# Kernel tuning notes

Measured on AMD Instinct MI355X. Metric: run time of the kernel, lower is better.

The kernel has to match this reference:

```python
import jax, jax.numpy as jnp
import numpy as np

N_NODES = 50000
N_EDGES = 800000
IN_FEATS = 128
OUT_FEATS = 128
ALPHA = 0.5
BETA = 0.5


def setup_inputs() -> dict:
    key = jax.random.key(0)
    k_feat, k_src, k_dst, k_w = jax.random.split(key, 4)
    feat = jax.random.normal(k_feat, (N_NODES, IN_FEATS), dtype=jnp.float32)
    src = jax.random.randint(k_src, (N_EDGES,), 0, N_NODES, dtype=jnp.int64)
    dst = jax.random.randint(k_dst, (N_EDGES,), 0, N_NODES, dtype=jnp.int64)
    # xavier_uniform init for weight, zeros for bias
    bound = float(np.sqrt(6.0 / (IN_FEATS + OUT_FEATS)))
    weight = jax.random.uniform(k_w, (IN_FEATS, OUT_FEATS), dtype=jnp.float32,
                                minval=-bound, maxval=bound)
    bias = jnp.zeros((OUT_FEATS,), dtype=jnp.float32)
    return {"feat": feat, "weight": weight, "bias": bias, "src": src, "dst": dst}


def reference(feat, weight, bias, src, dst):
    n = feat.shape[0]
    ones = jnp.ones(src.shape[0], dtype=feat.dtype)
    deg_out = jax.ops.segment_sum(ones, src, num_segments=n)  # out-degree per node
    deg_in = jax.ops.segment_sum(ones, dst, num_segments=n)   # in-degree per node
    deg_out = jnp.maximum(deg_out, 1.0)
    deg_in = jnp.maximum(deg_in, 1.0)
    # norm = deg_in^{-alpha} * deg_out^{-beta}, applied to source features
    norm = deg_in ** (-ALPHA) * deg_out ** (-BETA)  # [N]
    h = feat * norm[:, None]                        # [N, in]
    if IN_FEATS > OUT_FEATS:
        h = h @ weight                              # project first, then aggregate
        rst = jax.ops.segment_sum(h[src], dst, num_segments=n)
    else:
        rst = jax.ops.segment_sum(h[src], dst, num_segments=n)  # copy_u + sum SpMM
        rst = rst @ weight
    rst = rst + bias
    return jax.nn.relu(rst)
```

## Files before the change

kernel.cpp:

```cpp
#include <hip/hip_runtime.h>

#define NF 128
#define NCHUNK 32
#define NRH 4
#define NRF 8
#define NNW_MAX 25088
#define RWH_MAX ((NNW_MAX + NRH - 1) / NRH)
#define RWF_MAX ((NNW_MAX + NRF - 1) / NRF)
#define GG_NODES 16

typedef __attribute__((ext_vector_type(8))) short short8;
typedef __attribute__((ext_vector_type(4))) float f32x4;
typedef unsigned int uint;
typedef unsigned short ushort;

__device__ __forceinline__ ushort f2bf(float f) {
    uint u = __float_as_uint(f);
    uint r = (u + 0x7fffu + ((u >> 16) & 1u)) >> 16;
    return (ushort)r;
}
__device__ __forceinline__ float bflo(uint v) { return __uint_as_float(v << 16); }
__device__ __forceinline__ float bfhi(uint v) { return __uint_as_float(v & 0xffff0000u); }

__global__ __launch_bounds__(1024) void hist_kernel(const int* __restrict__ src,
                                                    const int* __restrict__ dst,
                                                    uint* __restrict__ partial_in,
                                                    uint* __restrict__ partial_out,
                                                    int n_edges, int nwords, int epb, int rw) {
    __shared__ uint h[RWH_MAX];
    int wbeg = blockIdx.z * rw;
    int wend = min(wbeg + rw, nwords);
    int nw = wend - wbeg;
    for (int w = threadIdx.x; w < nw; w += 1024) h[w] = 0;
    __syncthreads();
    const int* idx = blockIdx.y ? src : dst;
    int ebeg = blockIdx.x * epb;
    int eend = min(ebeg + epb, n_edges);
    int nodelo = wbeg * 2, nodehi = wend * 2;
    for (int e = ebeg + (int)threadIdx.x; e < eend; e += 1024) {
        int node = idx[e];
        if (node >= nodelo && node < nodehi)
            atomicAdd(&h[(node >> 1) - wbeg], 1u << ((node & 1) * 16));
    }
    __syncthreads();
    uint* p = (blockIdx.y ? partial_out : partial_in) + (size_t)blockIdx.x * nwords + wbeg;
    for (int w = threadIdx.x; w < nw; w += 1024) p[w] = h[w];
}

__global__ __launch_bounds__(512) void dnr_kernel(const uint* __restrict__ partial_in,
                                                  uint* __restrict__ partial_out,
                                                  int* __restrict__ deg_in,
                                                  float* __restrict__ norm,
                                                  int* __restrict__ bsum,
                                                  int nwords, int n) {
    int w = blockIdx.x * 512 + (int)threadIdx.x;
    uint si0 = 0, si1 = 0, so0 = 0, so1 = 0;
    if (w < nwords) {
        for (int c = 0; c < NCHUNK; ++c) {
            uint vi = partial_in[(size_t)c * nwords + w];
            uint vo = partial_out[(size_t)c * nwords + w];
            partial_out[(size_t)c * nwords + w] = si0 | (si1 << 16);
            si0 += vi & 0xffffu; si1 += vi >> 16;
            so0 += vo & 0xffffu; so1 += vo >> 16;
        }
        int n0 = 2 * w, n1 = 2 * w + 1;
        {
            uint di = si0 < 1u ? 1u : si0, dv = so0 < 1u ? 1u : so0;
            deg_in[n0] = (int)si0;
            norm[n0] = 1.0f / sqrtf((float)di * (float)dv);
        }
        if (n1 < n) {
            uint di = si1 < 1u ? 1u : si1, dv = so1 < 1u ? 1u : so1;
            deg_in[n1] = (int)si1;
            norm[n1] = 1.0f / sqrtf((float)di * (float)dv);
        }
    }
    int v = (int)(si0 + si1);
#pragma unroll
    for (int off = 32; off >= 1; off >>= 1) v += __shfl_down(v, off, 64);
    __shared__ int wsum[8];
    int wave = threadIdx.x >> 6, lane = threadIdx.x & 63;
    if (lane == 0) wsum[wave] = v;
    __syncthreads();
    if (threadIdx.x == 0) {
        int s = 0;
#pragma unroll
        for (int k = 0; k < 8; ++k) s += wsum[k];
        bsum[blockIdx.x] = s;
    }
}

__global__ __launch_bounds__(1024) void prepscan_kernel(const float* __restrict__ feat,
                                                        const float* __restrict__ norm,
                                                        uint* __restrict__ featn, int total,
                                                        const float* __restrict__ W,
                                                        uint* __restrict__ wt,
                                                        const int* __restrict__ deg,
                                                        const int* __restrict__ bsum,
                                                        int* __restrict__ start,
                                                        int n, int nb, int nfb4) {
    int bid = (int)blockIdx.x;
    if (bid < nfb4) {
        int idx = bid * 1024 + (int)threadIdx.x;
        if (idx < total) {
            int node = idx >> 6;
            float nv = norm[node];
            float2 v = ((const float2*)feat)[idx];
            featn[idx] = (uint)f2bf(v.x * nv) | ((uint)f2bf(v.y * nv) << 16);
        }
        return;
    }
    if (bid < nfb4 + 8) {
        int idx = (bid - nfb4) * 1024 + (int)threadIdx.x;
        if (idx < NF * NF / 2) {
            int nrow = idx >> 6;
            int k2 = idx & 63;
            float a = W[(2 * k2) * NF + nrow];
            float b = W[(2 * k2 + 1) * NF + nrow];
            wt[idx] = (uint)f2bf(a) | ((uint)f2bf(b) << 16);
        }
        return;
    }
    int b = bid - nfb4 - 8;
    if (b >= nb) return;
    __shared__ int ws[16];
    __shared__ int wo[16];
    __shared__ int bpre_s;
    int i = b * 1024 + (int)threadIdx.x;
    int v = (i < n) ? deg[i] : 0;
    int lane = threadIdx.x & 63, wv = threadIdx.x >> 6;
    int incl = v;
#pragma unroll
    for (int off = 1; off < 64; off <<= 1) {
        int t = __shfl_up(incl, off, 64);
        if (lane >= off) incl += t;
    }
    if (lane == 63) ws[wv] = incl;
    if (threadIdx.x < 64) {
        int bb = ((int)threadIdx.x < nb) ? bsum[threadIdx.x] : 0;
        int bi = bb;
#pragma unroll
        for (int off = 1; off < 64; off <<= 1) {
            int t = __shfl_up(bi, off, 64);
            if (lane >= off) bi += t;
        }
        int bex = bi - bb;
        int mine = __shfl(bex, b, 64);
        if (threadIdx.x == 0) bpre_s = mine;
    }
    __syncthreads();
    if (threadIdx.x == 0) {
        int s = 0;
#pragma unroll
        for (int k = 0; k < 16; ++k) { wo[k] = s; s += ws[k]; }
    }
    __syncthreads();
    if (i < n) start[i] = incl - v + wo[wv] + bpre_s;
}

__global__ __launch_bounds__(1024) void fill3_kernel(const int* __restrict__ src,
                                                     const int* __restrict__ dst,
                                                     const uint* __restrict__ rel,
                                                     const int* __restrict__ start,
                                                     int* __restrict__ csr_src,
                                                     int n_edges, int nwords, int epb, int rwf) {
    __shared__ uint cur[RWF_MAX];
    int c = blockIdx.x >> 3;
    int r = blockIdx.x & 7;
    int wbeg = r * rwf;
    int wend = min(wbeg + rwf, nwords);
    int nw = wend - wbeg;
    for (int w = threadIdx.x; w < nw; w += 1024) cur[w] = 0;
    __syncthreads();
    const uint* relc = rel + (size_t)c * nwords;
    int ebeg = c * epb;
    int eend = min(ebeg + epb, n_edges);
    int nodelo = wbeg * 2, nodehi = wend * 2;
    for (int e = ebeg + (int)threadIdx.x; e < eend; e += 1024) {
        int d = dst[e];
        if (d >= nodelo && d < nodehi) {
            int sh = (d & 1) * 16;
            uint old = atomicAdd(&cur[(d >> 1) - wbeg], 1u << sh);
            uint rank = (old >> sh) & 0xffffu;
            uint relv = (relc[d >> 1] >> sh) & 0xffffu;
            int pos = start[d] + (int)(relv + rank);
            csr_src[pos] = src[e];
        }
    }
}

__global__ __launch_bounds__(128) void gathergemm_kernel(const uint* __restrict__ featn,
                                                         const int* __restrict__ csr_src,
                                                         const int* __restrict__ start,
                                                         const int* __restrict__ deg,
                                                         const ushort* __restrict__ wt_h,
                                                         const float* __restrict__ bias,
                                                         float* __restrict__ out,
                                                         int n_nodes) {
    __shared__ uint rstl[GG_NODES][68];
    int wave = threadIdx.x >> 6;
    int lane = threadIdx.x & 63;
    int base = blockIdx.x * GG_NODES;
    if (base >= n_nodes) return;
    int half = lane >> 5;
    int hl   = lane & 31;

    for (int p = 0; p < 4; ++p) {
        int node = base + wave * 8 + p * 2 + half;
        int beg = 0, dg = 0;
        if (node < n_nodes) { beg = start[node]; dg = deg[node]; }
        const uint2* fp = (const uint2*)featn;
        float a0x = 0.f, a0y = 0.f, a1x = 0.f, a1y = 0.f;
        float b0x = 0.f, b0y = 0.f, b1x = 0.f, b1y = 0.f;
        int i = 0;
        for (; i + 7 < dg; i += 8) {
            int s0 = csr_src[beg + i];
            int s1 = csr_src[beg + i + 1];
            int s2 = csr_src[beg + i + 2];
            int s3 = csr_src[beg + i + 3];
            int s4 = csr_src[beg + i + 4];
            int s5 = csr_src[beg + i + 5];
            int s6 = csr_src[beg + i + 6];
            int s7 = csr_src[beg + i + 7];
            uint2 v0 = fp[(size_t)s0 * 32 + hl];
            uint2 v1 = fp[(size_t)s1 * 32 + hl];
            uint2 v2 = fp[(size_t)s2 * 32 + hl];
            uint2 v3 = fp[(size_t)s3 * 32 + hl];
            uint2 v4 = fp[(size_t)s4 * 32 + hl];
            uint2 v5 = fp[(size_t)s5 * 32 + hl];
            uint2 v6 = fp[(size_t)s6 * 32 + hl];
            uint2 v7 = fp[(size_t)s7 * 32 + hl];
            a0x += bflo(v0.x); a0y += bfhi(v0.x); a1x += bflo(v0.y); a1y += bfhi(v0.y);
            b0x += bflo(v1.x); b0y += bfhi(v1.x); b1x += bflo(v1.y); b1y += bfhi(v1.y);
            a0x += bflo(v2.x); a0y += bfhi(v2.x); a1x += bflo(v2.y); a1y += bfhi(v2.y);
            b0x += bflo(v3.x); b0y += bfhi(v3.x); b1x += bflo(v3.y); b1y += bfhi(v3.y);
            a0x += bflo(v4.x); a0y += bfhi(v4.x); a1x += bflo(v4.y); a1y += bfhi(v4.y);
            b0x += bflo(v5.x); b0y += bfhi(v5.x); b1x += bflo(v5.y); b1y += bfhi(v5.y);
            a0x += bflo(v6.x); a0y += bfhi(v6.x); a1x += bflo(v6.y); a1y += bfhi(v6.y);
            b0x += bflo(v7.x); b0y += bfhi(v7.x); b1x += bflo(v7.y); b1y += bfhi(v7.y);
        }
        for (; i + 1 < dg; i += 2) {
            int s0 = csr_src[beg + i];
            int s1 = csr_src[beg + i + 1];
            uint2 v0 = fp[(size_t)s0 * 32 + hl];
            uint2 v1 = fp[(size_t)s1 * 32 + hl];
            a0x += bflo(v0.x); a0y += bfhi(v0.x); a1x += bflo(v0.y); a1y += bfhi(v0.y);
            b0x += bflo(v1.x); b0y += bfhi(v1.x); b1x += bflo(v1.y); b1y += bfhi(v1.y);
        }
        if (i < dg) {
            int s = csr_src[beg + i];
            uint2 v = fp[(size_t)s * 32 + hl];
            a0x += bflo(v.x); a0y += bfhi(v.x); a1x += bflo(v.y); a1y += bfhi(v.y);
        }
        float r0x = a0x + b0x, r0y = a0y + b0y;
        float r1x = a1x + b1x, r1y = a1y + b1y;
        uint w0 = (uint)f2bf(r0x) | ((uint)f2bf(r0y) << 16);
        uint w1 = (uint)f2bf(r1x) | ((uint)f2bf(r1y) << 16);
        *(uint2*)&rstl[wave * 8 + p * 2 + half][hl * 2] = make_uint2(w0, w1);
    }
    __syncthreads();

    int l16 = lane & 15, lq = lane >> 4;
    int nt0 = wave * 4;

    short8 a[4];
#pragma unroll
    for (int kt = 0; kt < 4; ++kt)
        a[kt] = *(const short8*)&rstl[l16][kt * 16 + lq * 4];

#pragma unroll
    for (int t = 0; t < 4; ++t) {
        int nt = nt0 + t;
        f32x4 acc = {0.0f, 0.0f, 0.0f, 0.0f};
        const ushort* bp = wt_h + (size_t)(nt * 16 + l16) * NF + lq * 8;
#pragma unroll
        for (int kt = 0; kt < 4; ++kt) {
            short8 b = *(const short8*)(bp + kt * 32);
            acc = __builtin_amdgcn_mfma_f32_16x16x32_bf16(a[kt], b, acc, 0, 0, 0);
        }
        int col = nt * 16 + l16;
        float bv = bias[col];
#pragma unroll
        for (int r = 0; r < 4; ++r) {
            int orow = base + lq * 4 + r;
            if (orow < n_nodes) {
                float v = acc[r] + bv;
                out[(size_t)orow * NF + col] = v > 0.0f ? v : 0.0f;
            }
        }
    }
}

__global__ __launch_bounds__(256) void deg_kernel(const int* __restrict__ src,
                                                  const int* __restrict__ dst,
                                                  int* __restrict__ deg_out,
                                                  int* __restrict__ deg_in,
                                                  int n_edges) {
    int i = blockIdx.x * 256 + threadIdx.x;
    if (i < n_edges) {
        atomicAdd(&deg_out[src[i]], 1);
        atomicAdd(&deg_in[dst[i]], 1);
    }
}
__global__ __launch_bounds__(256) void norm_kernel(const int* __restrict__ deg_out,
                                                   const int* __restrict__ deg_in,
                                                   float* __restrict__ norm, int n) {
    int i = blockIdx.x * 256 + threadIdx.x;
    if (i < n) {
        int dov = deg_out[i]; if (dov < 1) dov = 1;
        int div_ = deg_in[i]; if (div_ < 1) div_ = 1;
        norm[i] = 1.0f / sqrtf((float)dov * (float)div_);
    }
}
__global__ __launch_bounds__(256) void prep_kernel(const float* __restrict__ feat,
                                                   const float* __restrict__ norm,
                                                   uint* __restrict__ featn, int total,
                                                   const float* __restrict__ W,
                                                   uint* __restrict__ wt, int nfb) {
    if ((int)blockIdx.x < nfb) {
        int idx = blockIdx.x * 256 + threadIdx.x;
        if (idx >= total) return;
        int node = idx >> 6;
        float nv = norm[node];
        float2 v = ((const float2*)feat)[idx];
        featn[idx] = (uint)f2bf(v.x * nv) | ((uint)f2bf(v.y * nv) << 16);
    } else {
        int idx = (blockIdx.x - nfb) * 256 + threadIdx.x;
        if (idx >= NF * NF / 2) return;
        int nrow = idx >> 6;
        int k2 = idx & 63;
        float a = W[(2 * k2) * NF + nrow];
        float b = W[(2 * k2 + 1) * NF + nrow];
        wt[idx] = (uint)f2bf(a) | ((uint)f2bf(b) << 16);
    }
}
__global__ __launch_bounds__(1024) void scan_sum_kernel(const int* __restrict__ deg,
                                                        int* __restrict__ bsum, int n) {
    int i = blockIdx.x * 1024 + threadIdx.x;
    int v = (i < n) ? deg[i] : 0;
#pragma unroll
    for (int off = 32; off >= 1; off >>= 1) v += __shfl_down(v, off, 64);
    __shared__ int ws[16];
    int wv = threadIdx.x >> 6, lane = threadIdx.x & 63;
    if (lane == 0) ws[wv] = v;
    __syncthreads();
    if (threadIdx.x == 0) {
        int s = 0;
#pragma unroll
        for (int k = 0; k < 16; ++k) s += ws[k];
        bsum[blockIdx.x] = s;
    }
}
__global__ __launch_bounds__(1024) void scan_bsum_kernel(int* __restrict__ bsum, int nb) {
    __shared__ int s[1024];
    int v = (threadIdx.x < (unsigned)nb) ? bsum[threadIdx.x] : 0;
    s[threadIdx.x] = v;
    __syncthreads();
    for (int off = 1; off < 1024; off <<= 1) {
        int t = (threadIdx.x >= (unsigned)off) ? s[threadIdx.x - off] : 0;
        __syncthreads();
        s[threadIdx.x] += t;
        __syncthreads();
    }
    if (threadIdx.x < (unsigned)nb) bsum[threadIdx.x] = s[threadIdx.x] - v;
}
__global__ __launch_bounds__(1024) void scan_final_kernel(const int* __restrict__ deg,
                                                          const int* __restrict__ bsum,
                                                          int* __restrict__ start,
                                                          int* __restrict__ cursor, int n) {
    int i = blockIdx.x * 1024 + threadIdx.x;
    int v = (i < n) ? deg[i] : 0;
    int lane = threadIdx.x & 63, wv = threadIdx.x >> 6;
    int incl = v;
#pragma unroll
    for (int off = 1; off < 64; off <<= 1) {
        int t = __shfl_up(incl, off, 64);
        if (lane >= off) incl += t;
    }
    __shared__ int ws[16];
    __shared__ int wo[16];
    if (lane == 63) ws[wv] = incl;
    __syncthreads();
    if (threadIdx.x == 0) {
        int s = 0;
#pragma unroll
        for (int k = 0; k < 16; ++k) { wo[k] = s; s += ws[k]; }
    }
    __syncthreads();
    int excl = incl - v + wo[wv] + bsum[blockIdx.x];
    if (i < n) { start[i] = excl; cursor[i] = excl; }
}
__global__ __launch_bounds__(256) void fill_kernel(const int* __restrict__ src,
                                                   const int* __restrict__ dst,
                                                   int* __restrict__ cursor,
                                                   int* __restrict__ csr_src,
                                                   int n_edges) {
    int e = blockIdx.x * 256 + threadIdx.x;
    if (e < n_edges) {
        int d = dst[e];
        int pos = atomicAdd(&cursor[d], 1);
        csr_src[pos] = src[e];
    }
}
__global__ __launch_bounds__(256) void gather_kernel(const uint* __restrict__ featn,
                                                     const int* __restrict__ csr_src,
                                                     const int* __restrict__ start,
                                                     const int* __restrict__ deg,
                                                     uint* __restrict__ rst_h,
                                                     int n_nodes) {
    int wid  = (blockIdx.x * 256 + threadIdx.x) >> 6;
    int lane = threadIdx.x & 63;
    if (wid >= n_nodes) return;
    int beg = start[wid];
    int end = beg + deg[wid];
    float ax = 0.f, ay = 0.f;
    for (int i = beg; i < end; ++i) {
        int s = csr_src[i];
        uint v = featn[(size_t)s * 64 + lane];
        ax += bflo(v); ay += bfhi(v);
    }
    rst_h[(size_t)wid * 64 + lane] = (uint)f2bf(ax) | ((uint)f2bf(ay) << 16);
}
__global__ __launch_bounds__(256) void gemm_mfma_kernel(const ushort* __restrict__ rst_h,
                                                        const ushort* __restrict__ wt_h,
                                                        const float* __restrict__ bias,
                                                        float* __restrict__ out,
                                                        int n_nodes) {
    int wave = threadIdx.x >> 6;
    int lane = threadIdx.x & 63;
    int row0 = blockIdx.x * 64 + wave * 16;
    if (row0 >= n_nodes) return;
    int l16 = lane & 15, lq = lane >> 4;
    short8 a[4];
    const ushort* ap = rst_h + (size_t)(row0 + l16) * NF + lq * 8;
#pragma unroll
    for (int kt = 0; kt < 4; ++kt) a[kt] = *(const short8*)(ap + kt * 32);
#pragma unroll
    for (int nt = 0; nt < 8; ++nt) {
        f32x4 acc = {0.0f, 0.0f, 0.0f, 0.0f};
        const ushort* bp = wt_h + (size_t)(nt * 16 + l16) * NF + lq * 8;
#pragma unroll
        for (int kt = 0; kt < 4; ++kt) {
            short8 b = *(const short8*)(bp + kt * 32);
            acc = __builtin_amdgcn_mfma_f32_16x16x32_bf16(a[kt], b, acc, 0, 0, 0);
        }
        int col = nt * 16 + l16;
        float bv = bias[col];
#pragma unroll
        for (int r = 0; r < 4; ++r) {
            int orow = row0 + lq * 4 + r;
            if (orow < n_nodes) {
                float v = acc[r] + bv;
                out[(size_t)orow * NF + col] = v > 0.0f ? v : 0.0f;
            }
        }
    }
}

extern "C" void kernel_launch(void* const* d_in, const int* in_sizes, int n_in,
                              void* d_out, int out_size, void* d_ws, size_t ws_size,
                              hipStream_t stream) {
    const float* feat = (const float*)d_in[0];
    const float* W    = (const float*)d_in[1];
    const float* bias = (const float*)d_in[2];
    const int*   src  = (const int*)d_in[3];
    const int*   dst  = (const int*)d_in[4];

    int n_nodes = in_sizes[0] / NF;
    int n_edges = in_sizes[3];

    char* ws = (char*)d_ws;
    size_t row_u32 = (size_t)n_nodes * 64;
    uint*  rst_h   = (uint*)ws;
    uint*  featn   = rst_h + row_u32;
    int*   deg_in  = (int*)(featn + row_u32);
    int*   deg_out = deg_in + n_nodes;
    float* norm    = (float*)(deg_out + n_nodes);
    int*   start   = (int*)(norm + n_nodes);
    int*   cursor  = start + n_nodes;
    int*   bsum    = cursor + n_nodes;
    uint*  wt      = (uint*)(bsum + 1024);
    int*   csr_src = (int*)(wt + NF * NF / 2);
    uint*  partial_in = (uint*)(csr_src + n_edges);

    int nwords = (n_nodes + 1) / 2;
    uint* partial_out = partial_in + (size_t)NCHUNK * nwords;
    size_t need = (size_t)((char*)(partial_out + (size_t)NCHUNK * nwords) - ws);

    int epb = (n_edges + NCHUNK - 1) / NCHUNK;
    int nb1024 = (n_nodes + 1023) / 1024;
    bool fast = (nwords <= NNW_MAX) && (epb < 65536) && (nb1024 <= 64) && (need <= ws_size);

    int total = n_nodes * 64;

    if (fast) {
        int rwh = (nwords + NRH - 1) / NRH;
        hist_kernel<<<dim3(NCHUNK, 2, NRH), 1024, 0, stream>>>(
            src, dst, partial_in, partial_out, n_edges, nwords, epb, rwh);
        dnr_kernel<<<nb1024, 512, 0, stream>>>(partial_in, partial_out, deg_in, norm,
                                               bsum, nwords, n_nodes);
        int nfb4 = (total + 1023) / 1024;
        prepscan_kernel<<<nfb4 + 8 + nb1024, 1024, 0, stream>>>(
            feat, norm, featn, total, W, wt, deg_in, bsum, start, n_nodes, nb1024, nfb4);
        int rwf = (nwords + NRF - 1) / NRF;
        fill3_kernel<<<NCHUNK * NRF, 1024, 0, stream>>>(src, dst, partial_out, start,
                                                        csr_src, n_edges, nwords, epb, rwf);
        gathergemm_kernel<<<(n_nodes + GG_NODES - 1) / GG_NODES, 128, 0, stream>>>(
            featn, csr_src, start, deg_in, (const ushort*)wt, bias, (float*)d_out, n_nodes);
    } else {
        int nfb = (total + 255) / 256;
        hipMemsetAsync(deg_in, 0, 2 * (size_t)n_nodes * sizeof(int), stream);
        deg_kernel<<<(n_edges + 255) / 256, 256, 0, stream>>>(src, dst, deg_out, deg_in, n_edges);
        norm_kernel<<<(n_nodes + 255) / 256, 256, 0, stream>>>(deg_out, deg_in, norm, n_nodes);
        prep_kernel<<<nfb + 32, 256, 0, stream>>>(feat, norm, featn, total, W, wt, nfb);
        int nb = (n_nodes + 1023) / 1024;
        scan_sum_kernel<<<nb, 1024, 0, stream>>>(deg_in, bsum, n_nodes);
        scan_bsum_kernel<<<1, 1024, 0, stream>>>(bsum, nb);
        scan_final_kernel<<<nb, 1024, 0, stream>>>(deg_in, bsum, start, cursor, n_nodes);
        fill_kernel<<<(n_edges + 255) / 256, 256, 0, stream>>>(src, dst, cursor, csr_src, n_edges);
        gather_kernel<<<(n_nodes * 64 + 255) / 256, 256, 0, stream>>>(featn, csr_src, start,
                                                                      deg_in, rst_h, n_nodes);
        gemm_mfma_kernel<<<(n_nodes + 63) / 64, 256, 0, stream>>>((const ushort*)rst_h,
                                                                  (const ushort*)wt, bias,
                                                                  (float*)d_out, n_nodes);
    }
}
```

Before: 93.81 us.

## Slice feature columns into four planes and split fused gather-GEMM into two kernels

Stores the normalized bf16 features as four column-slice planes of 32 features each. The gather runs one block per tile/slice pair, and each half-wave handles alternate edges for a slice, combining the halves with a shuffle. The idea is to shrink the gathered working set per slice so it stays cache resident and to give the gather more parallelism. The fused GEMM is replaced by a separate MFMA GEMM kernel that reads the sliced aggregate from global memory, which adds an extra launch and an intermediate write and read.

```diff
diff --git a/kernel.cpp b/kernel.cpp
--- a/kernel.cpp
+++ b/kernel.cpp
@@ -7,7 +7,8 @@
 #define NNW_MAX 25088
 #define RWH_MAX ((NNW_MAX + NRH - 1) / NRH)
 #define RWF_MAX ((NNW_MAX + NRF - 1) / NRF)
-#define GG_NODES 16
+#define GT_NODES 16
+#define NSL 4
 
 typedef __attribute__((ext_vector_type(8))) short short8;
 typedef __attribute__((ext_vector_type(4))) float f32x4;
@@ -103,9 +104,13 @@
     if (bid < nfb4) {
         int idx = bid * 1024 + (int)threadIdx.x;
         if (idx < total) {
-            int node = idx >> 6;
+            int spn = n * 16;
+            int slice = idx / spn;
+            int rem = idx - slice * spn;
+            int node = rem >> 4;
+            int u = rem & 15;
             float nv = norm[node];
-            float2 v = ((const float2*)feat)[idx];
+            float2 v = ((const float2*)feat)[node * 64 + slice * 16 + u];
             featn[idx] = (uint)f2bf(v.x * nv) | ((uint)f2bf(v.y * nv) << 16);
         }
         return;
@@ -189,88 +194,77 @@
     }
 }
 
-__global__ __launch_bounds__(128) void gathergemm_kernel(const uint* __restrict__ featn,
-                                                         const int* __restrict__ csr_src,
-                                                         const int* __restrict__ start,
-                                                         const int* __restrict__ deg,
-                                                         const ushort* __restrict__ wt_h,
-                                                         const float* __restrict__ bias,
-                                                         float* __restrict__ out,
-                                                         int n_nodes) {
-    __shared__ uint rstl[GG_NODES][68];
+__global__ __launch_bounds__(128) void gather_sl_kernel(const uint* __restrict__ featn,
+                                                        const int* __restrict__ csr_src,
+                                                        const int* __restrict__ start,
+                                                        const int* __restrict__ deg,
+                                                        uint* __restrict__ rst_sl,
+                                                        int n_nodes, int ntiles) {
+    int q = blockIdx.x & 7;
+    int tile = (blockIdx.x >> 3) * 2 + (q >> 2);
+    int slice = q & 3;
+    if (tile >= ntiles) return;
     int wave = threadIdx.x >> 6;
     int lane = threadIdx.x & 63;
-    int base = blockIdx.x * GG_NODES;
-    if (base >= n_nodes) return;
     int half = lane >> 5;
-    int hl   = lane & 31;
+    int hl = lane & 31;
+    int epair = hl >> 4;
+    int l16 = hl & 15;
+    const uint* fs = featn + (size_t)slice * n_nodes * 16;
 
     for (int p = 0; p < 4; ++p) {
-        int node = base + wave * 8 + p * 2 + half;
+        int node = tile * GT_NODES + wave * 8 + p * 2 + half;
         int beg = 0, dg = 0;
         if (node < n_nodes) { beg = start[node]; dg = deg[node]; }
-        const uint2* fp = (const uint2*)featn;
-        float a0x = 0.f, a0y = 0.f, a1x = 0.f, a1y = 0.f;
-        float b0x = 0.f, b0y = 0.f, b1x = 0.f, b1y = 0.f;
-        int i = 0;
-        for (; i + 7 < dg; i += 8) {
+        float ax0 = 0.f, ay0 = 0.f, ax1 = 0.f, ay1 = 0.f;
+        int i = epair;
+        for (; i + 6 < dg; i += 8) {
             int s0 = csr_src[beg + i];
-            int s1 = csr_src[beg + i + 1];
-            int s2 = csr_src[beg + i + 2];
-            int s3 = csr_src[beg + i + 3];
-            int s4 = csr_src[beg + i + 4];
-            int s5 = csr_src[beg + i + 5];
-            int s6 = csr_src[beg + i + 6];
-            int s7 = csr_src[beg + i + 7];
-            uint2 v0 = fp[(size_t)s0 * 32 + hl];
-            uint2 v1 = fp[(size_t)s1 * 32 + hl];
-            uint2 v2 = fp[(size_t)s2 * 32 + hl];
-            uint2 v3 = fp[(size_t)s3 * 32 + hl];
-            uint2 v4 = fp[(size_t)s4 * 32 + hl];
-            uint2 v5 = fp[(size_t)s5 * 32 + hl];
-            uint2 v6 = fp[(size_t)s6 * 32 + hl];
-            uint2 v7 = fp[(size_t)s7 * 32 + hl];
-            a0x += bflo(v0.x); a0y += bfhi(v0.x); a1x += bflo(v0.y); a1y += bfhi(v0.y);
-            b0x += bflo(v1.x); b0y += bfhi(v1.x); b1x += bflo(v1.y); b1y += bfhi(v1.y);
-            a0x += bflo(v2.x); a0y += bfhi(v2.x); a1x += bflo(v2.y); a1y += bfhi(v2.y);
-            b0x += bflo(v3.x); b0y += bfhi(v3.x); b1x += bflo(v3.y); b1y += bfhi(v3.y);
-            a0x += bflo(v4.x); a0y += bfhi(v4.x); a1x += bflo(v4.y); a1y += bfhi(v4.y);
-            b0x += bflo(v5.x); b0y += bfhi(v5.x); b1x += bflo(v5.y); b1y += bfhi(v5.y);
-            a0x += bflo(v6.x); a0y += bfhi(v6.x); a1x += bflo(v6.y); a1y += bfhi(v6.y);
-            b0x += bflo(v7.x); b0y += bfhi(v7.x); b1x += bflo(v7.y); b1y += bfhi(v7.y);
-        }
-        for (; i + 1 < dg; i += 2) {
-            int s0 = csr_src[beg + i];
-            int s1 = csr_src[beg + i + 1];
-            uint2 v0 = fp[(size_t)s0 * 32 + hl];
-            uint2 v1 = fp[(size_t)s1 * 32 + hl];
-            a0x += bflo(v0.x); a0y += bfhi(v0.x); a1x += bflo(v0.y); a1y += bfhi(v0.y);
-            b0x += bflo(v1.x); b0y += bfhi(v1.x); b1x += bflo(v1.y); b1y += bfhi(v1.y);
-        }
-        if (i < dg) {
+            int s1 = csr_src[beg + i + 2];
+            int s2 = csr_src[beg + i + 4];
+            int s3 = csr_src[beg + i + 6];
+            uint v0 = fs[(size_t)s0 * 16 + l16];
+            uint v1 = fs[(size_t)s1 * 16 + l16];
+            uint v2 = fs[(size_t)s2 * 16 + l16];
+            uint v3 = fs[(size_t)s3 * 16 + l16];
+            ax0 += bflo(v0); ay0 += bfhi(v0);
+            ax1 += bflo(v1); ay1 += bfhi(v1);
+            ax0 += bflo(v2); ay0 += bfhi(v2);
+            ax1 += bflo(v3); ay1 += bfhi(v3);
+        }
+        for (; i < dg; i += 2) {
             int s = csr_src[beg + i];
-            uint2 v = fp[(size_t)s * 32 + hl];
-            a0x += bflo(v.x); a0y += bfhi(v.x); a1x += bflo(v.y); a1y += bfhi(v.y);
-        }
-        float r0x = a0x + b0x, r0y = a0y + b0y;
-        float r1x = a1x + b1x, r1y = a1y + b1y;
-        uint w0 = (uint)f2bf(r0x) | ((uint)f2bf(r0y) << 16);
-        uint w1 = (uint)f2bf(r1x) | ((uint)f2bf(r1y) << 16);
-        *(uint2*)&rstl[wave * 8 + p * 2 + half][hl * 2] = make_uint2(w0, w1);
-    }
-    __syncthreads();
-
+            uint v = fs[(size_t)s * 16 + l16];
+            ax0 += bflo(v); ay0 += bfhi(v);
+        }
+        float ax = ax0 + ax1, ay = ay0 + ay1;
+        ax += __shfl_xor(ax, 16, 64);
+        ay += __shfl_xor(ay, 16, 64);
+        if (epair == 0 && node < n_nodes)
+            rst_sl[((size_t)slice * n_nodes + node) * 16 + l16] =
+                (uint)f2bf(ax) | ((uint)f2bf(ay) << 16);
+    }
+}
+
+__global__ __launch_bounds__(256) void gemm_sl_kernel(const ushort* __restrict__ rst_sl,
+                                                      const ushort* __restrict__ wt_h,
+                                                      const float* __restrict__ bias,
+                                                      float* __restrict__ out,
+                                                      int n_nodes) {
+    int wave = threadIdx.x >> 6;
+    int lane = threadIdx.x & 63;
+    int row0 = blockIdx.x * 64 + wave * 16;
+    if (row0 >= n_nodes) return;
     int l16 = lane & 15, lq = lane >> 4;
-    int nt0 = wave * 4;
+    int row = row0 + l16;
 
     short8 a[4];
 #pragma unroll
     for (int kt = 0; kt < 4; ++kt)
-        a[kt] = *(const short8*)&rstl[l16][kt * 16 + lq * 4];
-
-#pragma unroll
-    for (int t = 0; t < 4; ++t) {
-        int nt = nt0 + t;
+        a[kt] = *(const short8*)(rst_sl + ((size_t)kt * n_nodes + row) * 32 + lq * 8);
+
+#pragma unroll
+    for (int nt = 0; nt < 8; ++nt) {
         f32x4 acc = {0.0f, 0.0f, 0.0f, 0.0f};
         const ushort* bp = wt_h + (size_t)(nt * 16 + l16) * NF + lq * 8;
 #pragma unroll
@@ -282,7 +276,7 @@
         float bv = bias[col];
 #pragma unroll
         for (int r = 0; r < 4; ++r) {
-            int orow = base + lq * 4 + r;
+            int orow = row0 + lq * 4 + r;
             if (orow < n_nodes) {
                 float v = acc[r] + bv;
                 out[(size_t)orow * NF + col] = v > 0.0f ? v : 0.0f;
@@ -505,8 +499,12 @@
         int rwf = (nwords + NRF - 1) / NRF;
         fill3_kernel<<<NCHUNK * NRF, 1024, 0, stream>>>(src, dst, partial_out, start,
                                                         csr_src, n_edges, nwords, epb, rwf);
-        gathergemm_kernel<<<(n_nodes + GG_NODES - 1) / GG_NODES, 128, 0, stream>>>(
-            featn, csr_src, start, deg_in, (const ushort*)wt, bias, (float*)d_out, n_nodes);
+        int ntiles = (n_nodes + GT_NODES - 1) / GT_NODES;
+        int gblocks = ((ntiles + 1) / 2) * 8;
+        gather_sl_kernel<<<gblocks, 128, 0, stream>>>(featn, csr_src, start, deg_in,
+                                                      rst_h, n_nodes, ntiles);
+        gemm_sl_kernel<<<(n_nodes + 63) / 64, 256, 0, stream>>>(
+            (const ushort*)rst_h, (const ushort*)wt, bias, (float*)d_out, n_nodes);
     } else {
         int nfb = (total + 255) / 256;
         hipMemsetAsync(deg_in, 0, 2 * (size_t)n_nodes * sizeof(int), stream);
```

Measured after the change: 120.9 us. 1.29x slower.
